# Kernel tuning notes

Measured on AMD Instinct MI355X. Metric: run time of the kernel, lower is better.

## Reference

```python
import jax, jax.numpy as jnp
import numpy as np

B, L, D, K_LIN, T = 32, 512, 1024, 7, 8  # T = 1 identity ('root') + 7 linear experts


def setup_inputs() -> dict:
    key = jax.random.key(0)
    k0, k1, k2 = jax.random.split(key, 3)
    actions = jax.random.normal(k0, (B, L, D), dtype=jnp.float32)
    action_type = jax.random.randint(k1, (B, L), 0, T)
    W = jax.random.normal(k2, (K_LIN, D, D), dtype=jnp.float32) * 0.02  # (K, out, in)
    b = jnp.zeros((K_LIN, D), dtype=jnp.float32)
    return {"actions": actions, "action_type": action_type, "W": W, "b": b}


def reference(actions, action_type, W, b):
    # Project padded actions through ALL experts (matches original ModuleDict loop).
    # proj: (B, L, K_LIN, D) ; W is (K, out, in) so contract over input dim i.
    proj = jnp.einsum('bli,koi->blko', actions, W) + b[None, None, :, :]
    # 'root' expert is nn.Identity -> stacked first (dict insertion order).
    p = jnp.concatenate([actions[:, :, None, :], proj], axis=2)  # (B, L, T, D)
    # One-hot mask built via scatter in the original == one_hot here.
    mask = jax.nn.one_hot(action_type, T, dtype=p.dtype)[..., None]  # (B, L, T, 1)
    embedded = (mask * p).sum(axis=2)  # (B, L, D)
    return embedded
```

## Files before the change

### kernel.cpp

```cpp
#include <hip/hip_runtime.h>


#define NTOK 16384
#define DDIM 1024
#define NEXP 7
#define BM 256
#define BN 256
#define BK 64
#define NKT (DDIM / BK)
#define NYMAX 72

#define WI_OFFS   16
#define WI_NTILES 32
#define WI_TABLE  64
#define WI_CTOK   512
#define WI_SMAP   (512 + 16384)
#define WS_ABF_B  1048576
#define WS_WBF_B  (WS_ABF_B + NTOK * DDIM * 2)

typedef __attribute__((ext_vector_type(8))) short short8;
typedef __attribute__((ext_vector_type(4))) float f32x4;

__device__ __forceinline__ unsigned short f2bf(float f) {
    unsigned u = __float_as_uint(f);
    u += 0x7fff + ((u >> 16) & 1);
    return (unsigned short)(u >> 16);
}

__device__ __forceinline__ void gload16(const void* g, void* l) {
    __builtin_amdgcn_global_load_lds(
        (const __attribute__((address_space(1))) void*)g,
        (__attribute__((address_space(3))) void*)l, 16, 0, 0);
}

__global__ __launch_bounds__(1024) void route_k(
    const int* __restrict__ type, int* __restrict__ wsi) {
    __shared__ int h[16][8];
    __shared__ int cur[16][NEXP];
    const int tid = threadIdx.x, wave = tid >> 6;

    if (tid < 128) ((int*)h)[tid] = 0;
    __syncthreads();

    int kv[16];
#pragma unroll
    for (int i = 0; i < 16; ++i) {
        kv[i] = type[i * 1024 + tid];
        if (kv[i] > 0) atomicAdd(&h[wave][kv[i]], 1);
    }
    __syncthreads();

    if (tid == 0) {
        int acc = 0, t = 0;
        for (int e = 0; e < NEXP; ++e) {
            wsi[WI_OFFS + e] = acc;
            int run = acc;
            for (int w = 0; w < 16; ++w) { cur[w][e] = run; run += h[w][e + 1]; }
            int nt = (run - acc + BM - 1) >> 8;
            for (int i = 0; i < nt; ++i) {
                wsi[WI_TABLE + 2 * t] = e;
                wsi[WI_TABLE + 2 * t + 1] = acc + i * BM;
                ++t;
            }
            acc = run;
        }
        wsi[WI_OFFS + NEXP] = acc;
        wsi[WI_NTILES] = t;
    }
    __syncthreads();

#pragma unroll
    for (int i = 0; i < 16; ++i) {
        int t = i * 1024 + tid, s = -1;
        if (kv[i] > 0) {
            s = atomicAdd(&cur[wave][kv[i] - 1], 1);
            wsi[WI_CTOK + s] = t;
        }
        wsi[WI_SMAP + t] = s;
    }
}

__global__ __launch_bounds__(256) void fusedconv_k(
    const float* __restrict__ A, const int* __restrict__ wsi,
    const float* __restrict__ W, unsigned short* __restrict__ Wbf,
    unsigned short* __restrict__ Abf, float* __restrict__ out) {
    const int bid = blockIdx.x, tid = threadIdx.x;
    if (bid < 4096) {
        int wave = tid >> 6, lane = tid & 63;
        int t = bid * 4 + wave;
        int s = wsi[WI_SMAP + t];
        const float4* src = (const float4*)(A + (size_t)t * DDIM);
        if (s < 0) {
            float4* d = (float4*)(out + (size_t)t * DDIM);
#pragma unroll
            for (int j = 0; j < 4; ++j) d[lane + j * 64] = src[lane + j * 64];
        } else {
            float4 v0 = src[lane * 4 + 0], v1 = src[lane * 4 + 1];
            float4 v2 = src[lane * 4 + 2], v3 = src[lane * 4 + 3];
            short8 h0, h1;
            h0[0]=f2bf(v0.x); h0[1]=f2bf(v0.y); h0[2]=f2bf(v0.z); h0[3]=f2bf(v0.w);
            h0[4]=f2bf(v1.x); h0[5]=f2bf(v1.y); h0[6]=f2bf(v1.z); h0[7]=f2bf(v1.w);
            h1[0]=f2bf(v2.x); h1[1]=f2bf(v2.y); h1[2]=f2bf(v2.z); h1[3]=f2bf(v2.w);
            h1[4]=f2bf(v3.x); h1[5]=f2bf(v3.y); h1[6]=f2bf(v3.z); h1[7]=f2bf(v3.w);
            unsigned short* d = Abf + (size_t)s * DDIM + lane * 16;
            *(short8*)d = h0;
            *(short8*)(d + 8) = h1;
        }
    } else {
        size_t i = ((size_t)(bid - 4096) * 256 + tid) * 16;
        const float4* src = (const float4*)(W + i);
        float4 v0 = src[0], v1 = src[1], v2 = src[2], v3 = src[3];
        short8 h0, h1;
        h0[0]=f2bf(v0.x); h0[1]=f2bf(v0.y); h0[2]=f2bf(v0.z); h0[3]=f2bf(v0.w);
        h0[4]=f2bf(v1.x); h0[5]=f2bf(v1.y); h0[6]=f2bf(v1.z); h0[7]=f2bf(v1.w);
        h1[0]=f2bf(v2.x); h1[1]=f2bf(v2.y); h1[2]=f2bf(v2.z); h1[3]=f2bf(v2.w);
        h1[4]=f2bf(v3.x); h1[5]=f2bf(v3.y); h1[6]=f2bf(v3.z); h1[7]=f2bf(v3.w);
        *(short8*)(Wbf + i) = h0;
        *(short8*)(Wbf + i + 8) = h1;
    }
}

#define LDA8(CA, SL)                                               \
    _Pragma("unroll")                                              \
    for (int m = 0; m < 8; ++m)                                    \
        a8[m] = *(const short8*)((const char*)CA + wr * 16384 +    \
                                 lane15 * 128 + m * 2048 + (SL));

#define LDB2(CB, N0, SL)                                           \
    bA = *(const short8*)((const char*)CB + wc * 8192 +            \
                          lane15 * 128 + (N0) * 2048 + (SL));      \
    bB = *(const short8*)((const char*)CB + wc * 8192 +            \
                          lane15 * 128 + ((N0) + 1) * 2048 + (SL));

#define MFMA_PHASE(N0, N1)                                         \
    __builtin_amdgcn_s_barrier();                                  \
    asm volatile("s_waitcnt lgkmcnt(0)" ::: "memory");             \
    __builtin_amdgcn_sched_barrier(0);                             \
    __builtin_amdgcn_s_setprio(1);                                 \
    _Pragma("unroll")                                              \
    for (int m = 0; m < 8; ++m) {                                  \
        acc[m][N0] = __builtin_amdgcn_mfma_f32_16x16x32_bf16(      \
            a8[m], bA, acc[m][N0], 0, 0, 0);                       \
        acc[m][N1] = __builtin_amdgcn_mfma_f32_16x16x32_bf16(      \
            a8[m], bB, acc[m][N1], 0, 0, 0);                       \
    }                                                              \
    __builtin_amdgcn_s_setprio(0);                                 \
    __builtin_amdgcn_s_barrier();

#define KTILE(CA, CB, NA, NB, KT)                                  \
    do {                                                           \
        if ((KT) + 1 < NKT) {                                      \
            const int ke_ = ((KT) + 1) * BK;                       \
            _Pragma("unroll")                                      \
            for (int q = 0; q < 4; ++q)                            \
                gload16(aSrc[q] + ke_,                             \
                        (char*)NA + wave * 1024 + q * 8192);       \
            _Pragma("unroll")                                      \
            for (int q = 0; q < 4; ++q)                            \
                gload16(bSrc[q] + ke_,                             \
                        (char*)NB + wave * 1024 + q * 8192);       \
            asm volatile("s_waitcnt vmcnt(8)" ::: "memory");       \
        } else {                                                   \
            asm volatile("s_waitcnt vmcnt(0)" ::: "memory");       \
        }                                                          \
        __builtin_amdgcn_s_barrier();                              \
        {                                                          \
            short8 a8[8], bA, bB;                                  \
            LDA8(CA, sl0); LDB2(CB, 0, sl0);                       \
            MFMA_PHASE(0, 1);                                      \
            LDB2(CB, 2, sl0);                                      \
            MFMA_PHASE(2, 3);                                      \
            LDA8(CA, sl1); LDB2(CB, 2, sl1);                       \
            MFMA_PHASE(2, 3);                                      \
            LDB2(CB, 0, sl1);                                      \
            MFMA_PHASE(0, 1);                                      \
        }                                                          \
    } while (0)

__global__ __launch_bounds__(512, 2) void gemm_k(
    const unsigned short* __restrict__ Abf,
    const unsigned short* __restrict__ Wbf,
    const float* __restrict__ bias, float* __restrict__ out,
    const int* __restrict__ wsi) {
    const int bid = blockIdx.x;
    const int c = bid & 7, j = bid >> 3;
    const int ty = (j >> 2) * 8 + c;
    const int tx = j & 3;
    if (ty >= wsi[WI_NTILES]) return;
    const int* offs = wsi + WI_OFFS;
    const int* tab  = wsi + WI_TABLE;
    const int* ctok = wsi + WI_CTOK;
    const int e     = tab[2 * ty];
    const int crow0 = tab[2 * ty + 1];
    const int nend  = offs[e + 1];
    const int col0  = tx * BN;

    __shared__ unsigned short As0[BM * BK];
    __shared__ unsigned short As1[BM * BK];
    __shared__ unsigned short Bs0[BM * BK];
    __shared__ unsigned short Bs1[BM * BK];

    const int tid = threadIdx.x, lane = tid & 63, wave = tid >> 6;
    const int wr = wave >> 2, wc = wave & 3;
    const int lane15 = lane & 15;

    const int srow = lane >> 3;
    const int schunk = ((lane & 7) ^ srow) * 8;

    const unsigned short* Wb = Wbf + (size_t)e * DDIM * DDIM;
    const unsigned short* aSrc[4];
    const unsigned short* bSrc[4];
#pragma unroll
    for (int q = 0; q < 4; ++q) {
        int r = min(crow0 + q * 64 + wave * 8 + srow, NTOK - 1);
        aSrc[q] = Abf + (size_t)r * DDIM + schunk;
        bSrc[q] = Wb + (size_t)(col0 + q * 64 + wave * 8 + srow) * DDIM + schunk;
    }

    const int sl0 = (((lane >> 4)) ^ (lane & 7)) * 16;
    const int sl1 = ((4 | (lane >> 4)) ^ (lane & 7)) * 16;

    f32x4 acc[8][4];
#pragma unroll
    for (int m = 0; m < 8; ++m)
#pragma unroll
        for (int n = 0; n < 4; ++n) acc[m][n] = (f32x4){0.f, 0.f, 0.f, 0.f};

#pragma unroll
    for (int q = 0; q < 4; ++q)
        gload16(aSrc[q], (char*)As0 + wave * 1024 + q * 8192);
#pragma unroll
    for (int q = 0; q < 4; ++q)
        gload16(bSrc[q], (char*)Bs0 + wave * 1024 + q * 8192);

    for (int kt2 = 0; kt2 < NKT / 2; ++kt2) {
        KTILE(As0, Bs0, As1, Bs1, 2 * kt2);
        KTILE(As1, Bs1, As0, Bs0, 2 * kt2 + 1);
    }

    const int crow4 = (lane >> 4) * 4;
    float bv[4];
#pragma unroll
    for (int n = 0; n < 4; ++n)
        bv[n] = bias[e * DDIM + col0 + wc * 64 + n * 16 + lane15];

#pragma unroll
    for (int m = 0; m < 8; ++m) {
#pragma unroll
        for (int r = 0; r < 4; ++r) {
            int gr = crow0 + wr * 128 + m * 16 + crow4 + r;
            if (gr >= nend) continue;
            int tok = ctok[gr];
            float* orow = out + (size_t)tok * DDIM + col0 + wc * 64 + lane15;
#pragma unroll
            for (int n = 0; n < 4; ++n)
                orow[n * 16] = acc[m][n][r] + bv[n];
        }
    }
}

extern "C" void kernel_launch(void* const* d_in, const int* in_sizes, int n_in,
                              void* d_out, int out_size, void* d_ws, size_t ws_size,
                              hipStream_t stream) {
    const float* actions = (const float*)d_in[0];
    const int*   atype   = (const int*)d_in[1];
    const float* W       = (const float*)d_in[2];
    const float* bias    = (const float*)d_in[3];
    float* out = (float*)d_out;

    int* wsi = (int*)d_ws;
    unsigned short* Abf = (unsigned short*)((char*)d_ws + WS_ABF_B);
    unsigned short* Wbf = (unsigned short*)((char*)d_ws + WS_WBF_B);

    route_k<<<1, 1024, 0, stream>>>(atype, wsi);
    fusedconv_k<<<4096 + 1792, 256, 0, stream>>>(actions, wsi, W, Wbf, Abf, out);
    gemm_k<<<NYMAX * 4, 512, 0, stream>>>(Abf, Wbf, bias, out, wsi);
}
```

Baseline: 85.99 us.

## Restructure GEMM k-tile loop to one barrier per tile with full-B fragment loads

Replaces the four-phase k-tile body, which had barriers and lgkmcnt waits around each MFMA phase, with a two-half schedule. Each half loads all 8 A and 4 B fragments for one k-slice and issues 32 MFMAs. The next tile's global-to-LDS loads are issued before the MFMAs, and a single vmcnt(0) wait plus one barrier closes each tile. LDS base pointers are precomputed outside the loop. This aims to cut synchronization overhead and raise MFMA density, at the cost of more live fragment registers and no staggered waits on outstanding global loads.

```diff
diff --git a/kernel.cpp b/kernel.cpp
--- a/kernel.cpp
+++ b/kernel.cpp
@@ -120,61 +120,49 @@
     }
 }
 
-#define LDA8(CA, SL)                                               \
-    _Pragma("unroll")                                              \
-    for (int m = 0; m < 8; ++m)                                    \
-        a8[m] = *(const short8*)((const char*)CA + wr * 16384 +    \
-                                 lane15 * 128 + m * 2048 + (SL));
-
-#define LDB2(CB, N0, SL)                                           \
-    bA = *(const short8*)((const char*)CB + wc * 8192 +            \
-                          lane15 * 128 + (N0) * 2048 + (SL));      \
-    bB = *(const short8*)((const char*)CB + wc * 8192 +            \
-                          lane15 * 128 + ((N0) + 1) * 2048 + (SL));
-
-#define MFMA_PHASE(N0, N1)                                         \
-    __builtin_amdgcn_s_barrier();                                  \
-    asm volatile("s_waitcnt lgkmcnt(0)" ::: "memory");             \
-    __builtin_amdgcn_sched_barrier(0);                             \
-    __builtin_amdgcn_s_setprio(1);                                 \
-    _Pragma("unroll")                                              \
-    for (int m = 0; m < 8; ++m) {                                  \
-        acc[m][N0] = __builtin_amdgcn_mfma_f32_16x16x32_bf16(      \
-            a8[m], bA, acc[m][N0], 0, 0, 0);                       \
-        acc[m][N1] = __builtin_amdgcn_mfma_f32_16x16x32_bf16(      \
-            a8[m], bB, acc[m][N1], 0, 0, 0);                       \
-    }                                                              \
-    __builtin_amdgcn_s_setprio(0);                                 \
-    __builtin_amdgcn_s_barrier();
-
-#define KTILE(CA, CB, NA, NB, KT)                                  \
+#define TILE(Abase, Bbase, sNA, sNB, KT)                           \
     do {                                                           \
+        short8 a1[8], b1[4];                                       \
+        _Pragma("unroll")                                          \
+        for (int m = 0; m < 8; ++m)                                \
+            a1[m] = *(const short8*)(Abase + sl0 + m * 2048);      \
+        _Pragma("unroll")                                          \
+        for (int n = 0; n < 4; ++n)                                \
+            b1[n] = *(const short8*)(Bbase + sl0 + n * 2048);      \
         if ((KT) + 1 < NKT) {                                      \
             const int ke_ = ((KT) + 1) * BK;                       \
             _Pragma("unroll")                                      \
             for (int q = 0; q < 4; ++q)                            \
-                gload16(aSrc[q] + ke_,                             \
-                        (char*)NA + wave * 1024 + q * 8192);       \
+                gload16(aSrc[q] + ke_, sNA + q * 8192);            \
             _Pragma("unroll")                                      \
             for (int q = 0; q < 4; ++q)                            \
-                gload16(bSrc[q] + ke_,                             \
-                        (char*)NB + wave * 1024 + q * 8192);       \
-            asm volatile("s_waitcnt vmcnt(8)" ::: "memory");       \
-        } else {                                                   \
-            asm volatile("s_waitcnt vmcnt(0)" ::: "memory");       \
+                gload16(bSrc[q] + ke_, sNB + q * 8192);            \
         }                                                          \
+        __builtin_amdgcn_s_setprio(1);                             \
+        _Pragma("unroll")                                          \
+        for (int m = 0; m < 8; ++m)                                \
+            _Pragma("unroll")                                      \
+            for (int n = 0; n < 4; ++n)                            \
+                acc[m][n] = __builtin_amdgcn_mfma_f32_16x16x32_bf16(\
+                    a1[m], b1[n], acc[m][n], 0, 0, 0);             \
+        __builtin_amdgcn_s_setprio(0);                             \
+        short8 a2[8], b2[4];                                       \
+        _Pragma("unroll")                                          \
+        for (int m = 0; m < 8; ++m)                                \
+            a2[m] = *(const short8*)(Abase + sl1 + m * 2048);      \
+        _Pragma("unroll")                                          \
+        for (int n = 0; n < 4; ++n)                                \
+            b2[n] = *(const short8*)(Bbase + sl1 + n * 2048);      \
+        __builtin_amdgcn_s_setprio(1);                             \
+        _Pragma("unroll")                                          \
+        for (int m = 0; m < 8; ++m)                                \
+            _Pragma("unroll")                                      \
+            for (int n = 0; n < 4; ++n)                            \
+                acc[m][n] = __builtin_amdgcn_mfma_f32_16x16x32_bf16(\
+                    a2[m], b2[n], acc[m][n], 0, 0, 0);             \
+        __builtin_amdgcn_s_setprio(0);                             \
+        asm volatile("s_waitcnt vmcnt(0)" ::: "memory");           \
         __builtin_amdgcn_s_barrier();                              \
-        {                                                          \
-            short8 a8[8], bA, bB;                                  \
-            LDA8(CA, sl0); LDB2(CB, 0, sl0);                       \
-            MFMA_PHASE(0, 1);                                      \
-            LDB2(CB, 2, sl0);                                      \
-            MFMA_PHASE(2, 3);                                      \
-            LDA8(CA, sl1); LDB2(CB, 2, sl1);                       \
-            MFMA_PHASE(2, 3);                                      \
-            LDB2(CB, 0, sl1);                                      \
-            MFMA_PHASE(0, 1);                                      \
-        }                                                          \
     } while (0)
 
 __global__ __launch_bounds__(512, 2) void gemm_k(
@@ -219,6 +207,14 @@
 
     const int sl0 = (((lane >> 4)) ^ (lane & 7)) * 16;
     const int sl1 = ((4 | (lane >> 4)) ^ (lane & 7)) * 16;
+    const char* aR0 = (const char*)As0 + wr * 16384 + lane15 * 128;
+    const char* aR1 = (const char*)As1 + wr * 16384 + lane15 * 128;
+    const char* bR0 = (const char*)Bs0 + wc * 8192 + lane15 * 128;
+    const char* bR1 = (const char*)Bs1 + wc * 8192 + lane15 * 128;
+    char* sA0 = (char*)As0 + wave * 1024;
+    char* sA1 = (char*)As1 + wave * 1024;
+    char* sB0 = (char*)Bs0 + wave * 1024;
+    char* sB1 = (char*)Bs1 + wave * 1024;
 
     f32x4 acc[8][4];
 #pragma unroll
@@ -227,15 +223,15 @@
         for (int n = 0; n < 4; ++n) acc[m][n] = (f32x4){0.f, 0.f, 0.f, 0.f};
 
 #pragma unroll
-    for (int q = 0; q < 4; ++q)
-        gload16(aSrc[q], (char*)As0 + wave * 1024 + q * 8192);
-#pragma unroll
-    for (int q = 0; q < 4; ++q)
-        gload16(bSrc[q], (char*)Bs0 + wave * 1024 + q * 8192);
+    for (int q = 0; q < 4; ++q) gload16(aSrc[q], sA0 + q * 8192);
+#pragma unroll
+    for (int q = 0; q < 4; ++q) gload16(bSrc[q], sB0 + q * 8192);
+    asm volatile("s_waitcnt vmcnt(0)" ::: "memory");
+    __builtin_amdgcn_s_barrier();
 
     for (int kt2 = 0; kt2 < NKT / 2; ++kt2) {
-        KTILE(As0, Bs0, As1, Bs1, 2 * kt2);
-        KTILE(As1, Bs1, As0, Bs0, 2 * kt2 + 1);
+        TILE(aR0, bR0, sA1, sB1, 2 * kt2);
+        TILE(aR1, bR1, sA0, sB0, 2 * kt2 + 1);
     }
 
     const int crow4 = (lane >> 4) * 4;
```

Result: faster. 81.65 us (-5.1%).
